# Kernel optimization log

Hardware: AMD Instinct MI355X
Metric: run time of the kernel (lower is better)

The kernel has to match this reference:

```python
import jax, jax.numpy as jnp
import numpy as np

NUM_NODES = 100000
NUM_EDGES = 3_200_000
WALKS_PER_NODE = 4
WALK_LENGTH = 8
SKIP_FIRST = True


def setup_inputs() -> dict:
    key = jax.random.key(0)
    k1, k2, k3 = jax.random.split(key, 3)
    edge_index = jax.random.randint(k1, (2, NUM_EDGES), 0, NUM_NODES, dtype=jnp.int32)
    edge_weight = jax.random.uniform(k2, (NUM_EDGES,), dtype=jnp.float32)
    # one uniform per walker per step; S = NUM_NODES * WALKS_PER_NODE
    rand_unif = jax.random.uniform(k3, (NUM_NODES * WALKS_PER_NODE, WALK_LENGTH), dtype=jnp.float32)
    return {"edge_index": edge_index, "edge_weight": edge_weight, "rand_unif": rand_unif}


def _random_walk_edges(edge_index, rand_unif):
    """Returns added [2, S*L] edges (root -> walked node), int dtype."""
    row, col = edge_index[0], edge_index[1]
    # is_sorted=False path: sort edges by source to build CSR
    order = jnp.argsort(row)
    row_s = row[order]
    col_s = col[order]
    deg = jax.ops.segment_sum(jnp.ones_like(row_s), row_s, num_segments=NUM_NODES)  # [N]
    rowptr = jnp.concatenate([jnp.zeros((1,), deg.dtype), jnp.cumsum(deg)])  # [N+1]
    # start = all nodes, repeated walks_per_node times
    start = jnp.tile(jnp.arange(NUM_NODES, dtype=row.dtype), WALKS_PER_NODE)  # [S]

    def step(cur, u):
        d = deg[cur]  # [S]
        off = jnp.minimum((u * d.astype(u.dtype)).astype(cur.dtype), jnp.maximum(d - 1, 0))
        nxt = jnp.where(d > 0, col_s[rowptr[cur] + off], cur)  # stay if isolated
        return nxt, nxt

    _, walks = jax.lax.scan(step, start, rand_unif.T)  # [L_total, S]
    walks = walks.T  # [S, WALK_LENGTH] == n_id[:, 1:]
    k = 1 if SKIP_FIRST else 0  # skip_first drops the first-hop node (n_id[:, 2:])
    targets = walks[:, k:]  # [S, L]
    L = targets.shape[1]
    roots = jnp.broadcast_to(start[:, None], (start.shape[0], L))
    return jnp.stack([roots.reshape(-1), targets.reshape(-1)])  # [2, S*L]


def reference(edge_index, edge_weight, rand_unif):
    added = _random_walk_edges(edge_index, rand_unif)
    out_edge_index = jnp.concatenate([edge_index, added], axis=1)
    added_w = jnp.ones((added.shape[1],), edge_weight.dtype)
    out_edge_weight = jnp.concatenate([edge_weight, added_w])
    return out_edge_index, out_edge_weight
```

## Files before the change

kernel.cpp:

```cpp
#include <hip/hip_runtime.h>

#define ARW_N_NODES   100000
#define ARW_N_EDGES   3200000
#define ARW_N_WALKERS 400000
#define ARW_WLEN      8
#define ARW_LOUT      7
#define ARW_ROW_LEN   6000000
#define ARW_OUT_ELEMS 18000000

#define ARW_NB    256
#define ARW_RPB   392
#define ARW_NT    782
#define ARW_TP    784
#define ARW_TILE  4096
#define ARW_PMAX  14336

#define ARW_HT    0
#define ARW_BT    900000
#define ARW_TOT   1750000
#define ARW_CB    1760000
#define ARW_PD    1800000
#define ARW_P     6000000
#define ARW_COLS  12000000

__global__ void AddRandomWalkEdge_16896401342869_kernel() {}

__global__ __launch_bounds__(1024) void arw16896_thist(const int* __restrict__ row,
                                                       int* __restrict__ s) {
    __shared__ int h[256];
    int tid = threadIdx.x, t = blockIdx.x;
    if (tid < 256) h[tid] = 0;
    __syncthreads();
    #pragma unroll
    for (int rnd = 0; rnd < 4; rnd++) {
        int e = t * ARW_TILE + rnd * 1024 + tid;
        if (e < ARW_N_EDGES) atomicAdd(&h[row[e] / ARW_RPB], 1);
    }
    __syncthreads();
    if (tid < 256) s[ARW_HT + t * 256 + tid] = h[tid];
}

__global__ __launch_bounds__(1024) void arw16896_bscan2(int* __restrict__ s) {
    __shared__ int wsum[16];
    int b = blockIdx.x, tid = threadIdx.x, lane = tid & 63, wid = tid >> 6;
    int v = (tid < ARW_NT) ? s[ARW_HT + tid * 256 + b] : 0;
    int sv = v;
    #pragma unroll
    for (int off = 1; off < 64; off <<= 1) {
        int x = __shfl_up(sv, off, 64);
        if (lane >= off) sv += x;
    }
    if (lane == 63) wsum[wid] = sv;
    __syncthreads();
    int pre = 0, tot = 0;
    #pragma unroll
    for (int w = 0; w < 16; w++) {
        int x = wsum[w];
        if (w < wid) pre += x;
        tot += x;
    }
    if (tid < ARW_NT) s[ARW_BT + b * ARW_TP + tid] = pre + sv - v;
    if (tid == 0) s[ARW_TOT + b] = tot;
}

__global__ __launch_bounds__(256) void arw16896_bbase(int* __restrict__ s) {
    __shared__ int sm[256];
    int tid = threadIdx.x;
    int v = s[ARW_TOT + tid];
    sm[tid] = v;
    __syncthreads();
    for (int off = 1; off < 256; off <<= 1) {
        int x = 0;
        if (tid >= off) x = sm[tid - off];
        __syncthreads();
        sm[tid] += x;
        __syncthreads();
    }
    s[ARW_CB + tid] = sm[tid] - v;
}

__global__ __launch_bounds__(1024) void arw16896_part(const int* __restrict__ row,
                                                      const int* __restrict__ col,
                                                      int* __restrict__ s) {
    __shared__ unsigned short W[16 * 256];
    __shared__ int runc[256], lbase[256];
    int tid  = threadIdx.x;
    int wave = tid >> 6, lane = tid & 63;
    int t = blockIdx.x;
    if (tid < 256) {
        runc[tid]  = 0;
        lbase[tid] = s[ARW_CB + tid] + s[ARW_BT + tid * ARW_TP + t];
    }
    __syncthreads();
    #pragma unroll
    for (int rnd = 0; rnd < 4; rnd++) {
        int e = t * ARW_TILE + rnd * 1024 + tid;
        int valid = (e < ARW_N_EDGES) ? 1 : 0;
        int r = valid ? row[e] : 0;
        int cv = valid ? col[e] : 0;
        int b = r / ARW_RPB;
        int lr = r - b * ARW_RPB;
        #pragma unroll
        for (int j = 0; j < 4; j++) W[tid + j * 1024] = 0;
        __syncthreads();
        unsigned long long mask = ~0ULL;
        #pragma unroll
        for (int bit = 0; bit < 8; bit++) {
            unsigned long long bal = __ballot((b >> bit) & 1);
            mask &= ((b >> bit) & 1) ? bal : ~bal;
        }
        mask &= __ballot(valid);
        int rankw = __popcll(mask & ((1ULL << lane) - 1ULL));
        if (valid) W[wave * 256 + b] = (unsigned short)__popcll(mask);
        __syncthreads();
        if (valid) {
            int cross = 0;
            for (int w2 = 0; w2 < 16; w2++) {
                if (w2 >= wave) break;
                cross += (int)W[w2 * 256 + b];
            }
            s[ARW_P + lbase[b] + runc[b] + cross + rankw] = (lr << 17) | cv;
        }
        __syncthreads();
        if (tid < 256) {
            int a = 0;
            #pragma unroll
            for (int w = 0; w < 16; w++) a += (int)W[w * 256 + tid];
            runc[tid] += a;
        }
        __syncthreads();
    }
}

__global__ __launch_bounds__(1024) void arw16896_pass2(int* __restrict__ s) {
    __shared__ int PL[ARW_PMAX];
    __shared__ unsigned short W[16 * 512];
    __shared__ int hist[512], pref[512], runc[512];
    int tid = threadIdx.x, lane = tid & 63, wave = tid >> 6;
    int b = blockIdx.x;
    int start = s[ARW_CB + b];
    int end   = (b == ARW_NB - 1) ? ARW_N_EDGES : s[ARW_CB + b + 1];
    int cnt = end - start;
    int staged = cnt < ARW_PMAX ? cnt : ARW_PMAX;
    int rows0 = b * ARW_RPB;
    int nrows = ARW_N_NODES - rows0; if (nrows > ARW_RPB) nrows = ARW_RPB;

    for (int k = tid; k < staged; k += 1024) PL[k] = s[ARW_P + start + k];
    if (tid < 512) hist[tid] = 0;
    __syncthreads();

    for (int k = tid; k < cnt; k += 1024) {
        unsigned p = (unsigned)(k < staged ? PL[k] : s[ARW_P + start + k]);
        atomicAdd(&hist[p >> 17], 1);
    }
    __syncthreads();
    if (tid < 512) pref[tid] = hist[tid];
    __syncthreads();
    for (int off = 1; off < 512; off <<= 1) {
        int x = 0;
        if (tid < 512 && tid >= off) x = pref[tid - off];
        __syncthreads();
        if (tid < 512) pref[tid] += x;
        __syncthreads();
    }
    if (tid < 512) runc[tid] = 0;
    if (tid < nrows) {
        unsigned deg = (unsigned)hist[tid];
        unsigned rp  = (unsigned)(start + pref[tid] - hist[tid]);
        s[ARW_PD + rows0 + tid] = (int)((rp << 10) | deg);
    }
    __syncthreads();

    for (int c0 = 0; c0 < cnt; c0 += 1024) {
        int k = c0 + tid;
        int valid = (k < cnt) ? 1 : 0;
        unsigned p = 0u;
        if (valid) p = (unsigned)(k < staged ? PL[k] : s[ARW_P + start + k]);
        unsigned lr = p >> 17;
        #pragma unroll
        for (int j = 0; j < 8; j++) W[tid + j * 1024] = 0;
        __syncthreads();
        unsigned long long mask = ~0ULL;
        #pragma unroll
        for (int bit = 0; bit < 9; bit++) {
            unsigned long long bal = __ballot((lr >> bit) & 1u);
            mask &= ((lr >> bit) & 1u) ? bal : ~bal;
        }
        mask &= __ballot(valid);
        int rankw = __popcll(mask & ((1ULL << lane) - 1ULL));
        if (valid) W[wave * 512 + lr] = (unsigned short)__popcll(mask);
        __syncthreads();
        if (valid) {
            int cross = 0;
            for (int w2 = 0; w2 < 16; w2++) {
                if (w2 >= wave) break;
                cross += (int)W[w2 * 512 + lr];
            }
            int pos = start + (pref[lr] - hist[lr]) + runc[lr] + cross + rankw;
            s[ARW_COLS + pos] = (int)(p & 0x1FFFFu);
        }
        __syncthreads();
        if (tid < 512) {
            int a = 0;
            #pragma unroll
            for (int w = 0; w < 16; w++) a += (int)W[w * 512 + tid];
            runc[tid] += a;
        }
        __syncthreads();
    }
}

__global__ __launch_bounds__(256) void arw16896_walk(const float* __restrict__ ru,
                                                     const int* __restrict__ ei,
                                                     const int* __restrict__ s,
                                                     float* __restrict__ o) {
    __shared__ float tg[4 * 256 * ARW_LOUT];
    int tid = threadIdx.x;
    int v = blockIdx.x * 256 + tid;
    if (v < ARW_N_NODES) {
        float uu[4][8];
        int cur[4];
        #pragma unroll
        for (int k = 0; k < 4; k++) {
            const float4* rp4 = (const float4*)(ru + (size_t)(v + k * ARW_N_NODES) * 8);
            float4 ra = rp4[0], rb = rp4[1];
            uu[k][0] = ra.x; uu[k][1] = ra.y; uu[k][2] = ra.z; uu[k][3] = ra.w;
            uu[k][4] = rb.x; uu[k][5] = rb.y; uu[k][6] = rb.z; uu[k][7] = rb.w;
        }
        unsigned pd0 = (unsigned)s[ARW_PD + v];
        int d0  = (int)(pd0 & 1023u);
        int rp0 = (int)(pd0 >> 10);
        #pragma unroll
        for (int k = 0; k < 4; k++) {
            int off = (int)(uu[k][0] * (float)d0);
            if (off > d0 - 1) off = d0 - 1;
            int nxt = s[ARW_COLS + rp0 + off];
            cur[k] = (d0 > 0) ? nxt : v;
        }
        #pragma unroll
        for (int t = 1; t < ARW_WLEN; t++) {
            unsigned pdk[4];
            #pragma unroll
            for (int k = 0; k < 4; k++) pdk[k] = (unsigned)s[ARW_PD + cur[k]];
            #pragma unroll
            for (int k = 0; k < 4; k++) {
                int d = (int)(pdk[k] & 1023u);
                int off = (int)(uu[k][t] * (float)d);
                if (off > d - 1) off = d - 1;
                int nxt = s[ARW_COLS + (int)(pdk[k] >> 10) + off];
                cur[k] = (d > 0) ? nxt : cur[k];
                tg[k * (256 * ARW_LOUT) + tid * ARW_LOUT + (t - 1)] = (float)cur[k];
            }
        }
    }
    __syncthreads();
    int blkN = ARW_N_NODES - blockIdx.x * 256;
    if (blkN > 256) blkN = 256;
    int valid = blkN * ARW_LOUT;
    #pragma unroll
    for (int k = 0; k < 4; k++) {
        int base = ARW_ROW_LEN + ARW_N_EDGES +
                   (k * ARW_N_NODES + blockIdx.x * 256) * ARW_LOUT;
        for (int j = tid; j < valid; j += 256)
            o[base + j] = tg[k * (256 * ARW_LOUT) + j];
    }
    int gid = blockIdx.x * 256 + tid;
    int stride = gridDim.x * 256;
    for (int i4 = gid; i4 < ARW_N_EDGES / 4; i4 += stride) {
        int4 r1 = ((const int4*)(ei + ARW_N_EDGES))[i4];
        ((float4*)(o + ARW_ROW_LEN))[i4] =
            make_float4((float)r1.x, (float)r1.y, (float)r1.z, (float)r1.w);
    }
    for (int i4 = gid; i4 < (ARW_N_WALKERS * ARW_LOUT) / 4; i4 += stride) {
        int i = i4 * 4;
        float4 r;
        r.x = (float)(((i    ) / ARW_LOUT) % ARW_N_NODES);
        r.y = (float)(((i + 1) / ARW_LOUT) % ARW_N_NODES);
        r.z = (float)(((i + 2) / ARW_LOUT) % ARW_N_NODES);
        r.w = (float)(((i + 3) / ARW_LOUT) % ARW_N_NODES);
        ((float4*)(o + ARW_N_EDGES))[i4] = r;
    }
}

__global__ __launch_bounds__(256) void arw16896_asm(const int* __restrict__ ei,
                                                    const float* __restrict__ wgt,
                                                    float* __restrict__ o) {
    int i4 = blockIdx.x * blockDim.x + threadIdx.x;
    if (i4 < ARW_N_EDGES / 4) {
        int4 r0 = ((const int4*)ei)[i4];
        float4 wv = ((const float4*)wgt)[i4];
        ((float4*)o)[i4] = make_float4((float)r0.x, (float)r0.y, (float)r0.z, (float)r0.w);
        ((float4*)(o + 2 * ARW_ROW_LEN))[i4] = wv;
    }
    if (i4 < (ARW_N_WALKERS * ARW_LOUT) / 4) {
        ((float4*)(o + 2 * ARW_ROW_LEN + ARW_N_EDGES))[i4] = make_float4(1.f, 1.f, 1.f, 1.f);
    }
}

extern "C" void kernel_launch(void* const* d_in, const int* in_sizes, int n_in,
                              void* d_out, int out_size, void* d_ws, size_t ws_size,
                              hipStream_t stream) {
    const int*   ei  = (const int*)d_in[0];
    const float* wgt = (const float*)d_in[1];
    const float* ru  = (const float*)d_in[2];
    int*   s = (int*)d_out;
    float* o = (float*)d_out;
    const int* row = ei;
    const int* col = ei + ARW_N_EDGES;

    arw16896_thist <<<ARW_NT, 1024, 0, stream>>>(row, s);
    arw16896_bscan2<<<ARW_NB, 1024, 0, stream>>>(s);
    arw16896_bbase <<<1, 256, 0, stream>>>(s);
    arw16896_part  <<<ARW_NT, 1024, 0, stream>>>(row, col, s);
    arw16896_pass2 <<<ARW_NB, 1024, 0, stream>>>(s);
    arw16896_walk  <<<(ARW_N_NODES + 255) / 256, 256, 0, stream>>>(ru, ei, s, o);
    arw16896_asm   <<<(ARW_N_EDGES / 4 + 255) / 256, 256, 0, stream>>>(ei, wgt, o);
}
```

Before: 228.4 us.

## Fuse CSR-build kernels into one cooperative kernel with grid syncs

Merges the five CSR construction kernels (tile histogram, bucket scan, base scan, partition, per-bucket sort) into a single cooperative kernel of 256 blocks that loops over tiles and separates phases with grid.sync(). The base prefix scan is recomputed redundantly in each block's shared memory instead of going through global memory, and shared memory is reused through a union. This removes launch gaps and inter-kernel drains, but the histogram and partition phases now run with only 256 blocks doing about 3 tiles each, which lowers parallelism, and the grid barriers add their own cost.

```diff
diff --git a/kernel.cpp b/kernel.cpp
--- a/kernel.cpp
+++ b/kernel.cpp
@@ -1,4 +1,7 @@
 #include <hip/hip_runtime.h>
+#include <hip/hip_cooperative_groups.h>
+
+namespace cg = cooperative_groups;
 
 #define ARW_N_NODES   100000
 #define ARW_N_EDGES   3200000
@@ -18,195 +21,198 @@
 #define ARW_HT    0
 #define ARW_BT    900000
 #define ARW_TOT   1750000
-#define ARW_CB    1760000
 #define ARW_PD    1800000
 #define ARW_P     6000000
 #define ARW_COLS  12000000
 
 __global__ void AddRandomWalkEdge_16896401342869_kernel() {}
 
-__global__ __launch_bounds__(1024) void arw16896_thist(const int* __restrict__ row,
+__global__ __launch_bounds__(1024) void arw16896_fused(const int* __restrict__ row,
+                                                       const int* __restrict__ col,
                                                        int* __restrict__ s) {
-    __shared__ int h[256];
-    int tid = threadIdx.x, t = blockIdx.x;
-    if (tid < 256) h[tid] = 0;
-    __syncthreads();
-    #pragma unroll
-    for (int rnd = 0; rnd < 4; rnd++) {
-        int e = t * ARW_TILE + rnd * 1024 + tid;
-        if (e < ARW_N_EDGES) atomicAdd(&h[row[e] / ARW_RPB], 1);
-    }
-    __syncthreads();
-    if (tid < 256) s[ARW_HT + t * 256 + tid] = h[tid];
-}
-
-__global__ __launch_bounds__(1024) void arw16896_bscan2(int* __restrict__ s) {
+    cg::grid_group grid = cg::this_grid();
+    __shared__ union {
+        int h[256];
+        struct { unsigned short W[16 * 256]; int runc[256]; int lbase[256]; } d;
+        struct { int PL[ARW_PMAX]; unsigned short W[16 * 512];
+                 int hist[512], pref[512], runc[512]; } e;
+    } U;
+    __shared__ int cbL[257];
     __shared__ int wsum[16];
-    int b = blockIdx.x, tid = threadIdx.x, lane = tid & 63, wid = tid >> 6;
-    int v = (tid < ARW_NT) ? s[ARW_HT + tid * 256 + b] : 0;
-    int sv = v;
-    #pragma unroll
-    for (int off = 1; off < 64; off <<= 1) {
-        int x = __shfl_up(sv, off, 64);
-        if (lane >= off) sv += x;
-    }
-    if (lane == 63) wsum[wid] = sv;
-    __syncthreads();
-    int pre = 0, tot = 0;
-    #pragma unroll
-    for (int w = 0; w < 16; w++) {
-        int x = wsum[w];
-        if (w < wid) pre += x;
-        tot += x;
-    }
-    if (tid < ARW_NT) s[ARW_BT + b * ARW_TP + tid] = pre + sv - v;
-    if (tid == 0) s[ARW_TOT + b] = tot;
-}
-
-__global__ __launch_bounds__(256) void arw16896_bbase(int* __restrict__ s) {
-    __shared__ int sm[256];
-    int tid = threadIdx.x;
-    int v = s[ARW_TOT + tid];
-    sm[tid] = v;
-    __syncthreads();
-    for (int off = 1; off < 256; off <<= 1) {
-        int x = 0;
-        if (tid >= off) x = sm[tid - off];
-        __syncthreads();
-        sm[tid] += x;
-        __syncthreads();
-    }
-    s[ARW_CB + tid] = sm[tid] - v;
-}
-
-__global__ __launch_bounds__(1024) void arw16896_part(const int* __restrict__ row,
-                                                      const int* __restrict__ col,
-                                                      int* __restrict__ s) {
-    __shared__ unsigned short W[16 * 256];
-    __shared__ int runc[256], lbase[256];
-    int tid  = threadIdx.x;
-    int wave = tid >> 6, lane = tid & 63;
-    int t = blockIdx.x;
-    if (tid < 256) {
-        runc[tid]  = 0;
-        lbase[tid] = s[ARW_CB + tid] + s[ARW_BT + tid * ARW_TP + t];
-    }
-    __syncthreads();
-    #pragma unroll
-    for (int rnd = 0; rnd < 4; rnd++) {
-        int e = t * ARW_TILE + rnd * 1024 + tid;
-        int valid = (e < ARW_N_EDGES) ? 1 : 0;
-        int r = valid ? row[e] : 0;
-        int cv = valid ? col[e] : 0;
-        int b = r / ARW_RPB;
-        int lr = r - b * ARW_RPB;
-        #pragma unroll
-        for (int j = 0; j < 4; j++) W[tid + j * 1024] = 0;
-        __syncthreads();
-        unsigned long long mask = ~0ULL;
-        #pragma unroll
-        for (int bit = 0; bit < 8; bit++) {
-            unsigned long long bal = __ballot((b >> bit) & 1);
-            mask &= ((b >> bit) & 1) ? bal : ~bal;
-        }
-        mask &= __ballot(valid);
-        int rankw = __popcll(mask & ((1ULL << lane) - 1ULL));
-        if (valid) W[wave * 256 + b] = (unsigned short)__popcll(mask);
-        __syncthreads();
-        if (valid) {
-            int cross = 0;
-            for (int w2 = 0; w2 < 16; w2++) {
-                if (w2 >= wave) break;
-                cross += (int)W[w2 * 256 + b];
-            }
-            s[ARW_P + lbase[b] + runc[b] + cross + rankw] = (lr << 17) | cv;
-        }
-        __syncthreads();
+    int tid = threadIdx.x, lane = tid & 63, wave = tid >> 6;
+    int bid = blockIdx.x;
+
+    for (int t = bid; t < ARW_NT; t += ARW_NB) {
+        if (tid < 256) U.h[tid] = 0;
+        __syncthreads();
+        #pragma unroll
+        for (int rnd = 0; rnd < 4; rnd++) {
+            int e = t * ARW_TILE + rnd * 1024 + tid;
+            if (e < ARW_N_EDGES) atomicAdd(&U.h[row[e] / ARW_RPB], 1);
+        }
+        __syncthreads();
+        if (tid < 256) s[ARW_HT + t * 256 + tid] = U.h[tid];
+        __syncthreads();
+    }
+    grid.sync();
+
+    {
+        int v = (tid < ARW_NT) ? s[ARW_HT + tid * 256 + bid] : 0;
+        int sv = v;
+        #pragma unroll
+        for (int off = 1; off < 64; off <<= 1) {
+            int x = __shfl_up(sv, off, 64);
+            if (lane >= off) sv += x;
+        }
+        if (lane == 63) wsum[wave] = sv;
+        __syncthreads();
+        int pre = 0, tot = 0;
+        #pragma unroll
+        for (int w = 0; w < 16; w++) {
+            int x = wsum[w];
+            if (w < wave) pre += x;
+            tot += x;
+        }
+        if (tid < ARW_NT) s[ARW_BT + bid * ARW_TP + tid] = pre + sv - v;
+        if (tid == 0) s[ARW_TOT + bid] = tot;
+    }
+    grid.sync();
+
+    {
+        int v = (tid < 256) ? s[ARW_TOT + tid] : 0;
+        if (tid < 256) cbL[tid] = v;
+        __syncthreads();
+        for (int off = 1; off < 256; off <<= 1) {
+            int x = 0;
+            if (tid < 256 && tid >= off) x = cbL[tid - off];
+            __syncthreads();
+            if (tid < 256) cbL[tid] += x;
+            __syncthreads();
+        }
+        if (tid < 256) cbL[tid] -= v;
+        if (tid == 0) cbL[256] = ARW_N_EDGES;
+        __syncthreads();
+    }
+
+    for (int t = bid; t < ARW_NT; t += ARW_NB) {
         if (tid < 256) {
-            int a = 0;
-            #pragma unroll
-            for (int w = 0; w < 16; w++) a += (int)W[w * 256 + tid];
-            runc[tid] += a;
-        }
-        __syncthreads();
-    }
-}
-
-__global__ __launch_bounds__(1024) void arw16896_pass2(int* __restrict__ s) {
-    __shared__ int PL[ARW_PMAX];
-    __shared__ unsigned short W[16 * 512];
-    __shared__ int hist[512], pref[512], runc[512];
-    int tid = threadIdx.x, lane = tid & 63, wave = tid >> 6;
-    int b = blockIdx.x;
-    int start = s[ARW_CB + b];
-    int end   = (b == ARW_NB - 1) ? ARW_N_EDGES : s[ARW_CB + b + 1];
-    int cnt = end - start;
-    int staged = cnt < ARW_PMAX ? cnt : ARW_PMAX;
-    int rows0 = b * ARW_RPB;
-    int nrows = ARW_N_NODES - rows0; if (nrows > ARW_RPB) nrows = ARW_RPB;
-
-    for (int k = tid; k < staged; k += 1024) PL[k] = s[ARW_P + start + k];
-    if (tid < 512) hist[tid] = 0;
-    __syncthreads();
-
-    for (int k = tid; k < cnt; k += 1024) {
-        unsigned p = (unsigned)(k < staged ? PL[k] : s[ARW_P + start + k]);
-        atomicAdd(&hist[p >> 17], 1);
-    }
-    __syncthreads();
-    if (tid < 512) pref[tid] = hist[tid];
-    __syncthreads();
-    for (int off = 1; off < 512; off <<= 1) {
-        int x = 0;
-        if (tid < 512 && tid >= off) x = pref[tid - off];
-        __syncthreads();
-        if (tid < 512) pref[tid] += x;
-        __syncthreads();
-    }
-    if (tid < 512) runc[tid] = 0;
-    if (tid < nrows) {
-        unsigned deg = (unsigned)hist[tid];
-        unsigned rp  = (unsigned)(start + pref[tid] - hist[tid]);
-        s[ARW_PD + rows0 + tid] = (int)((rp << 10) | deg);
-    }
-    __syncthreads();
-
-    for (int c0 = 0; c0 < cnt; c0 += 1024) {
-        int k = c0 + tid;
-        int valid = (k < cnt) ? 1 : 0;
-        unsigned p = 0u;
-        if (valid) p = (unsigned)(k < staged ? PL[k] : s[ARW_P + start + k]);
-        unsigned lr = p >> 17;
-        #pragma unroll
-        for (int j = 0; j < 8; j++) W[tid + j * 1024] = 0;
-        __syncthreads();
-        unsigned long long mask = ~0ULL;
-        #pragma unroll
-        for (int bit = 0; bit < 9; bit++) {
-            unsigned long long bal = __ballot((lr >> bit) & 1u);
-            mask &= ((lr >> bit) & 1u) ? bal : ~bal;
-        }
-        mask &= __ballot(valid);
-        int rankw = __popcll(mask & ((1ULL << lane) - 1ULL));
-        if (valid) W[wave * 512 + lr] = (unsigned short)__popcll(mask);
-        __syncthreads();
-        if (valid) {
-            int cross = 0;
-            for (int w2 = 0; w2 < 16; w2++) {
-                if (w2 >= wave) break;
-                cross += (int)W[w2 * 512 + lr];
-            }
-            int pos = start + (pref[lr] - hist[lr]) + runc[lr] + cross + rankw;
-            s[ARW_COLS + pos] = (int)(p & 0x1FFFFu);
-        }
-        __syncthreads();
-        if (tid < 512) {
-            int a = 0;
-            #pragma unroll
-            for (int w = 0; w < 16; w++) a += (int)W[w * 512 + tid];
-            runc[tid] += a;
-        }
-        __syncthreads();
+            U.d.runc[tid]  = 0;
+            U.d.lbase[tid] = cbL[tid] + s[ARW_BT + tid * ARW_TP + t];
+        }
+        __syncthreads();
+        #pragma unroll
+        for (int rnd = 0; rnd < 4; rnd++) {
+            int e = t * ARW_TILE + rnd * 1024 + tid;
+            int valid = (e < ARW_N_EDGES) ? 1 : 0;
+            int r = valid ? row[e] : 0;
+            int cv = valid ? col[e] : 0;
+            int b = r / ARW_RPB;
+            int lr = r - b * ARW_RPB;
+            #pragma unroll
+            for (int j = 0; j < 4; j++) U.d.W[tid + j * 1024] = 0;
+            __syncthreads();
+            unsigned long long mask = ~0ULL;
+            #pragma unroll
+            for (int bit = 0; bit < 8; bit++) {
+                unsigned long long bal = __ballot((b >> bit) & 1);
+                mask &= ((b >> bit) & 1) ? bal : ~bal;
+            }
+            mask &= __ballot(valid);
+            int rankw = __popcll(mask & ((1ULL << lane) - 1ULL));
+            if (valid) U.d.W[wave * 256 + b] = (unsigned short)__popcll(mask);
+            __syncthreads();
+            if (valid) {
+                int cross = 0;
+                for (int w2 = 0; w2 < 16; w2++) {
+                    if (w2 >= wave) break;
+                    cross += (int)U.d.W[w2 * 256 + b];
+                }
+                s[ARW_P + U.d.lbase[b] + U.d.runc[b] + cross + rankw] = (lr << 17) | cv;
+            }
+            __syncthreads();
+            if (tid < 256) {
+                int a = 0;
+                #pragma unroll
+                for (int w = 0; w < 16; w++) a += (int)U.d.W[w * 256 + tid];
+                U.d.runc[tid] += a;
+            }
+            __syncthreads();
+        }
+    }
+    grid.sync();
+
+    {
+        int b = bid;
+        int start = cbL[b];
+        int end   = cbL[b + 1];
+        int cnt = end - start;
+        int staged = cnt < ARW_PMAX ? cnt : ARW_PMAX;
+        int rows0 = b * ARW_RPB;
+        int nrows = ARW_N_NODES - rows0; if (nrows > ARW_RPB) nrows = ARW_RPB;
+
+        for (int k = tid; k < staged; k += 1024) U.e.PL[k] = s[ARW_P + start + k];
+        if (tid < 512) U.e.hist[tid] = 0;
+        __syncthreads();
+
+        for (int k = tid; k < cnt; k += 1024) {
+            unsigned p = (unsigned)(k < staged ? U.e.PL[k] : s[ARW_P + start + k]);
+            atomicAdd(&U.e.hist[p >> 17], 1);
+        }
+        __syncthreads();
+        if (tid < 512) U.e.pref[tid] = U.e.hist[tid];
+        __syncthreads();
+        for (int off = 1; off < 512; off <<= 1) {
+            int x = 0;
+            if (tid < 512 && tid >= off) x = U.e.pref[tid - off];
+            __syncthreads();
+            if (tid < 512) U.e.pref[tid] += x;
+            __syncthreads();
+        }
+        if (tid < 512) U.e.runc[tid] = 0;
+        if (tid < nrows) {
+            unsigned deg = (unsigned)U.e.hist[tid];
+            unsigned rp  = (unsigned)(start + U.e.pref[tid] - U.e.hist[tid]);
+            s[ARW_PD + rows0 + tid] = (int)((rp << 10) | deg);
+        }
+        __syncthreads();
+
+        for (int c0 = 0; c0 < cnt; c0 += 1024) {
+            int k = c0 + tid;
+            int valid = (k < cnt) ? 1 : 0;
+            unsigned p = 0u;
+            if (valid) p = (unsigned)(k < staged ? U.e.PL[k] : s[ARW_P + start + k]);
+            unsigned lr = p >> 17;
+            #pragma unroll
+            for (int j = 0; j < 8; j++) U.e.W[tid + j * 1024] = 0;
+            __syncthreads();
+            unsigned long long mask = ~0ULL;
+            #pragma unroll
+            for (int bit = 0; bit < 9; bit++) {
+                unsigned long long bal = __ballot((lr >> bit) & 1u);
+                mask &= ((lr >> bit) & 1u) ? bal : ~bal;
+            }
+            mask &= __ballot(valid);
+            int rankw = __popcll(mask & ((1ULL << lane) - 1ULL));
+            if (valid) U.e.W[wave * 512 + lr] = (unsigned short)__popcll(mask);
+            __syncthreads();
+            if (valid) {
+                int cross = 0;
+                for (int w2 = 0; w2 < 16; w2++) {
+                    if (w2 >= wave) break;
+                    cross += (int)U.e.W[w2 * 512 + lr];
+                }
+                int pos = start + (U.e.pref[lr] - U.e.hist[lr]) + U.e.runc[lr] + cross + rankw;
+                s[ARW_COLS + pos] = (int)(p & 0x1FFFFu);
+            }
+            __syncthreads();
+            if (tid < 512) {
+                int a = 0;
+                #pragma unroll
+                for (int w = 0; w < 16; w++) a += (int)U.e.W[w * 512 + tid];
+                U.e.runc[tid] += a;
+            }
+            __syncthreads();
+        }
     }
 }
 
@@ -308,11 +314,9 @@
     const int* row = ei;
     const int* col = ei + ARW_N_EDGES;
 
-    arw16896_thist <<<ARW_NT, 1024, 0, stream>>>(row, s);
-    arw16896_bscan2<<<ARW_NB, 1024, 0, stream>>>(s);
-    arw16896_bbase <<<1, 256, 0, stream>>>(s);
-    arw16896_part  <<<ARW_NT, 1024, 0, stream>>>(row, col, s);
-    arw16896_pass2 <<<ARW_NB, 1024, 0, stream>>>(s);
-    arw16896_walk  <<<(ARW_N_NODES + 255) / 256, 256, 0, stream>>>(ru, ei, s, o);
-    arw16896_asm   <<<(ARW_N_EDGES / 4 + 255) / 256, 256, 0, stream>>>(ei, wgt, o);
+    void* fargs[] = { (void*)&row, (void*)&col, (void*)&s };
+    hipLaunchCooperativeKernel(reinterpret_cast<void*>(arw16896_fused),
+                               dim3(ARW_NB), dim3(1024), fargs, 0, stream);
+    arw16896_walk <<<(ARW_N_NODES + 255) / 256, 256, 0, stream>>>(ru, ei, s, o);
+    arw16896_asm  <<<(ARW_N_EDGES / 4 + 255) / 256, 256, 0, stream>>>(ei, wgt, o);
 }
```

After: 348.1 us. 52.4% more time.
